# Kernel tuning notes

Hardware: AMD Instinct MI355X
Metric: run time of the kernel (lower is better)

## Reference

```python
import jax, jax.numpy as jnp
import numpy as np

DIM = 128     # channels c (== LayerNorm dim); divisible by HEADS so qk_dim == dim
HEADS = 4
HIDDEN = 256  # dim * mlp_ratio (2.0)
B, H, W = 4, 128, 128


def setup_inputs() -> dict:
    key = jax.random.key(0)
    ks = jax.random.split(key, 8)
    d, hd = DIM, HIDDEN
    return {
        "x": jax.random.normal(ks[0], (B, d, H, W), jnp.float32),
        "ln1_g": jnp.ones((d,), jnp.float32),
        "ln1_b": jnp.zeros((d,), jnp.float32),
        "w_qkv": jax.random.normal(ks[1], (d, 3 * d), jnp.float32) * 0.02,
        "w_out": jax.random.normal(ks[2], (d, d), jnp.float32) * 0.02,
        "b_out": jnp.zeros((d,), jnp.float32),
        "ln2_g": jnp.ones((d,), jnp.float32),
        "ln2_b": jnp.zeros((d,), jnp.float32),
        "w_p0": jax.random.normal(ks[3], (d, hd), jnp.float32) * 0.02,
        "b_p0": jnp.zeros((hd,), jnp.float32),
        "dw_k": jax.random.normal(ks[4], (hd, 1, 5, 5), jnp.float32) * 0.1,
        "bn_g": jnp.ones((hd,), jnp.float32),
        "bn_b": jnp.zeros((hd,), jnp.float32),
        "w_p2": jax.random.normal(ks[5], (hd, d), jnp.float32) * 0.02,
        "b_p2": jnp.zeros((d,), jnp.float32),
        "region_size": 16,
    }


def _ln(x, g, b, eps=1e-5):
    m = x.mean(-1, keepdims=True)
    v = ((x - m) ** 2).mean(-1, keepdims=True)
    return (x - m) * jax.lax.rsqrt(v + eps) * g + b


def _forward(x, ln1_g, ln1_b, w_qkv, w_out, b_out, ln2_g, ln2_b,
             w_p0, b_p0, dw_k, bn_g, bn_b, w_p2, b_p2, region_size):
    b, c, h, w = x.shape
    rs = int(region_size)
    step = rs - 2
    # H,W chosen so pad_h = pad_w = 0 and (H - rs) % step == 0 -> full coverage
    n_r = (h - rs) // step + 1                      # regions per spatial axis (9)
    n = n_r * n_r                                   # total regions (81)
    starts = jnp.arange(n_r) * step
    hh = starts[:, None] + jnp.arange(rs)           # (n_r, rs) row indices
    ih = hh[:, None, :, None]                       # (n_r,1,rs,1)
    iw = hh[None, :, None, :]                       # (1,n_r,1,rs)

    # --- RegionPartitioner: overlapping windowed gather ---
    reg = x[:, :, ih, iw]                           # (b,c,n_r,n_r,rs,rs)
    # rearrange 'b n c h w -> (b n) (h w) c'
    tok = reg.transpose(0, 2, 3, 4, 5, 1).reshape(b * n, rs * rs, c)

    # --- PreNorm AdaptiveAttention + residual ---
    y = _ln(tok, ln1_g, ln1_b)
    qkv = y @ w_qkv                                 # (bn, s, 3c)
    q, k, v = jnp.split(qkv, 3, axis=-1)
    hd = c // HEADS
    split = lambda t: t.reshape(b * n, rs * rs, HEADS, hd).transpose(0, 2, 1, 3)
    q, k, v = split(q), split(k), split(v)
    attn = jax.nn.softmax(jnp.einsum('bhqd,bhkd->bhqk', q, k) * (hd ** -0.5), axis=-1)
    o = jnp.einsum('bhqk,bhkd->bhqd', attn, v)
    o = o.transpose(0, 2, 1, 3).reshape(b * n, rs * rs, c)
    tok = (o @ w_out + b_out) + tok

    # --- RegionIntegrator: overlap-add scatter + count normalize ---
    reg2 = tok.reshape(b, n_r, n_r, rs, rs, c).transpose(0, 5, 1, 2, 3, 4)  # (b,c,nr,nr,rs,rs)
    out = jnp.zeros((b, c, h, w), x.dtype).at[:, :, ih, iw].add(reg2)
    cnt = jnp.zeros((h, w), x.dtype).at[ih, iw].add(
        jnp.ones((n_r, n_r, rs, rs), x.dtype))
    merged = out / jnp.clip(cnt, 1e-8, None)[None, None]

    # --- PreNorm ConvMLP + residual ---
    xf = merged.transpose(0, 2, 3, 1).reshape(b, h * w, c)
    y = _ln(xf, ln2_g, ln2_b)
    y = y @ w_p0 + b_p0                              # (b, hw, hidden)
    ym = y.transpose(0, 2, 1).reshape(b, HIDDEN, h, w)
    ym = jax.lax.conv_general_dilated(
        ym, dw_k, window_strides=(1, 1), padding=[(2, 2), (2, 2)],
        feature_group_count=HIDDEN, dimension_numbers=('NCHW', 'OIHW', 'NCHW'))
    # BatchNorm2d (training-mode batch statistics, biased var, eps=1e-5)
    mu = ym.mean(axis=(0, 2, 3), keepdims=True)
    var = ((ym - mu) ** 2).mean(axis=(0, 2, 3), keepdims=True)
    ym = (ym - mu) * jax.lax.rsqrt(var + 1e-5) * bn_g[None, :, None, None] + bn_b[None, :, None, None]
    ym = jax.nn.gelu(ym, approximate=False)
    y = ym.reshape(b, HIDDEN, h * w).transpose(0, 2, 1)
    y = jax.nn.gelu(y, approximate=False)           # proj[1]
    y = y @ w_p2 + b_p2                              # proj[2]
    y = y + xf
    return y.reshape(b, h, w, c).transpose(0, 3, 1, 2)


def reference(x, ln1_g, ln1_b, w_qkv, w_out, b_out, ln2_g, ln2_b,
              w_p0, b_p0, dw_k, bn_g, bn_b, w_p2, b_p2, region_size):
    return _forward(x, ln1_g, ln1_b, w_qkv, w_out, b_out, ln2_g, ln2_b,
                    w_p0, b_p0, dw_k, bn_g, bn_b, w_p2, b_p2, region_size)
```

## Files before the change

### kernel.cpp

```cpp
#include <hip/hip_runtime.h>

#define DIMC 128
#define NHEADS 4
#define HD 32
#define HID 256
#define BB 4
#define HH_ 128
#define WW_ 128
#define HW 16384
#define RS 16
#define STEP 14
#define NR 9
#define NREGB 81
#define NREG 324
#define TT 256

typedef unsigned short bfu;
typedef __attribute__((ext_vector_type(8))) short bf16x8;
typedef __attribute__((ext_vector_type(4))) float f32x4;

__device__ __forceinline__ float bf2f(bfu u) {
  return __uint_as_float(((unsigned int)u) << 16);
}
__device__ __forceinline__ unsigned cvt_pk_bf16(float lo, float hi) {
  unsigned r;
  asm("v_cvt_pk_bf16_f32 %0, %1, %2" : "=v"(r) : "v"(lo), "v"(hi));
  return r;
}
__device__ __forceinline__ float gelu_fast(float x) {
  float x2 = x * x;
  float z = x * fmaf(x2, 0.07135481627f, 1.5957691216f);
  float e = __expf(-z);
  return __fdividef(x, 1.0f + e);
}

__global__ __launch_bounds__(256) void k1_gather(
    const float* __restrict__ x, const float* __restrict__ g,
    const float* __restrict__ bia, bfu* __restrict__ tok,
    bfu* __restrict__ aln, const float* __restrict__ wqkv,
    const float* __restrict__ wp0, const float* __restrict__ wp2,
    const float* __restrict__ wout, bfu* __restrict__ wqkvT,
    bfu* __restrict__ ap0, bfu* __restrict__ ap2, bfu* __restrict__ awout,
    float* __restrict__ bnacc) {
  int bid = blockIdx.x;
  int tid = threadIdx.x;
  if (bid >= NREG) {
    int pb = bid - NREG;
    if (pb < 24) {
      int task = pb * 256 + tid;
      int kg = task / 384, n = task % 384;
      float v[8];
      #pragma unroll
      for (int j = 0; j < 8; ++j) v[j] = wqkv[(kg * 8 + j) * 384 + n];
      uint4 pk = make_uint4(cvt_pk_bf16(v[0], v[1]), cvt_pk_bf16(v[2], v[3]),
                            cvt_pk_bf16(v[4], v[5]), cvt_pk_bf16(v[6], v[7]));
      *(uint4*)&wqkvT[(size_t)kg * 3072 + n * 8] = pk;
    } else if (pb == 24) {
      bnacc[tid] = 0.f;
      bnacc[256 + tid] = 0.f;
    } else if (pb < 41) {
      int task = (pb - 25) * 256 + tid;
      int kg = task >> 8, f = task & 255;
      float v[8];
      #pragma unroll
      for (int j = 0; j < 8; ++j) v[j] = wp0[(kg * 8 + j) * 256 + f];
      uint4 pk = make_uint4(cvt_pk_bf16(v[0], v[1]), cvt_pk_bf16(v[2], v[3]),
                            cvt_pk_bf16(v[4], v[5]), cvt_pk_bf16(v[6], v[7]));
      *(uint4*)&ap0[((size_t)kg * 256 + f) * 8] = pk;
    } else if (pb < 57) {
      int task = (pb - 41) * 256 + tid;
      int kg = task >> 7, c = task & 127;
      float v[8];
      #pragma unroll
      for (int j = 0; j < 8; ++j) v[j] = wp2[(kg * 8 + j) * 128 + c];
      uint4 pk = make_uint4(cvt_pk_bf16(v[0], v[1]), cvt_pk_bf16(v[2], v[3]),
                            cvt_pk_bf16(v[4], v[5]), cvt_pk_bf16(v[6], v[7]));
      *(uint4*)&ap2[((size_t)kg * 128 + c) * 8] = pk;
    } else {
      int task = (pb - 57) * 256 + tid;
      int kg = task >> 7, c = task & 127;
      float v[8];
      #pragma unroll
      for (int j = 0; j < 8; ++j) v[j] = wout[(kg * 8 + j) * 128 + c];
      uint4 pk = make_uint4(cvt_pk_bf16(v[0], v[1]), cvt_pk_bf16(v[2], v[3]),
                            cvt_pk_bf16(v[4], v[5]), cvt_pk_bf16(v[6], v[7]));
      *(uint4*)&awout[((size_t)kg * 128 + c) * 8] = pk;
    }
    return;
  }
  int reg = bid;
  int b = reg / NREGB, ij = reg % NREGB;
  int i = ij / NR, j = ij % NR;
  int t = tid;
  int r = t >> 4, s = t & 15;
  int hh = i * STEP + r, ww = j * STEP + s;
  const float* xp = x + (size_t)b * DIMC * HW + (size_t)hh * WW_ + ww;
  bfu* tp = tok + (size_t)reg * DIMC * TT + t;
  float sum = 0.f, sq = 0.f;
  #pragma unroll 4
  for (int c = 0; c < DIMC; c += 2) {
    float v0 = xp[(size_t)c * HW];
    float v1 = xp[(size_t)(c + 1) * HW];
    unsigned pk = cvt_pk_bf16(v0, v1);
    tp[c * TT] = (bfu)pk;
    tp[(c + 1) * TT] = (bfu)(pk >> 16);
    sum += v0 + v1;
    sq = fmaf(v0, v0, sq);
    sq = fmaf(v1, v1, sq);
  }
  float mu = sum * (1.0f / DIMC);
  float var = sq * (1.0f / DIMC) - mu * mu;
  float rstd = rsqrtf(var + 1e-5f);
  bfu* ap = aln + (size_t)reg * 32768 + t * 8;
  #pragma unroll
  for (int gidx = 0; gidx < 16; ++gidx) {
    float y[8];
    #pragma unroll
    for (int jj = 0; jj < 8; ++jj) {
      int c = gidx * 8 + jj;
      float vv = xp[(size_t)c * HW];
      y[jj] = (vv - mu) * rstd * g[c] + bia[c];
    }
    uint4 pk = make_uint4(cvt_pk_bf16(y[0], y[1]), cvt_pk_bf16(y[2], y[3]),
                          cvt_pk_bf16(y[4], y[5]), cvt_pk_bf16(y[6], y[7]));
    *(uint4*)&ap[(size_t)gidx * 2048] = pk;
  }
}

__global__ __launch_bounds__(256) void k23_fused(
    const bfu* __restrict__ aln, const bfu* __restrict__ wqkvT,
    bfu* __restrict__ o) {
  int reg = blockIdx.x;
  int h = blockIdx.y;
  __shared__ __align__(16) bfu sQ[256 * 40];
  __shared__ __align__(16) bfu sK[256 * 40];
  __shared__ __align__(16) bfu vperm[8 * 4 * 264];
  int tid = threadIdx.x;
  int wave = tid >> 6, lane = tid & 63;
  int quad = lane >> 4, n16 = lane & 15;

  const bfu* ab = aln + (size_t)reg * 32768 + (wave * 64 + n16) * 8;
  int colb[6];
  colb[0] = h * 32;
  colb[1] = h * 32 + 16;
  colb[2] = 128 + h * 32;
  colb[3] = 144 + h * 32;
  colb[4] = 256 + h * 32;
  colb[5] = 272 + h * 32;
  f32x4 acc[4][6];
  #pragma unroll
  for (int m = 0; m < 4; ++m)
    #pragma unroll
    for (int nt = 0; nt < 6; ++nt) acc[m][nt] = (f32x4){0.f, 0.f, 0.f, 0.f};
  #pragma unroll
  for (int ph = 0; ph < 4; ++ph) {
    int gg = ph * 4 + quad;
    bf16x8 af[4];
    #pragma unroll
    for (int m = 0; m < 4; ++m)
      af[m] = *(const bf16x8*)&ab[(size_t)gg * 2048 + m * 128];
    const bfu* bgg = wqkvT + (size_t)gg * 3072;
    bf16x8 bfr[6];
    #pragma unroll
    for (int nt = 0; nt < 6; ++nt)
      bfr[nt] = *(const bf16x8*)&bgg[(colb[nt] + n16) * 8];
    #pragma unroll
    for (int m = 0; m < 4; ++m)
      #pragma unroll
      for (int nt = 0; nt < 6; ++nt)
        acc[m][nt] =
            __builtin_amdgcn_mfma_f32_16x16x32_bf16(af[m], bfr[nt], acc[m][nt], 0, 0, 0);
  }
  #pragma unroll
  for (int m = 0; m < 4; ++m) {
    int g = wave * 2 + (m >> 1);
    int jt = (m & 1) * 4;
    int T0 = wave * 64 + m * 16 + quad * 4;
    unsigned q00 = cvt_pk_bf16(acc[m][0][0], acc[m][0][1]);
    unsigned q01 = cvt_pk_bf16(acc[m][0][2], acc[m][0][3]);
    unsigned q10 = cvt_pk_bf16(acc[m][1][0], acc[m][1][1]);
    unsigned q11 = cvt_pk_bf16(acc[m][1][2], acc[m][1][3]);
    unsigned k00 = cvt_pk_bf16(acc[m][2][0], acc[m][2][1]);
    unsigned k01 = cvt_pk_bf16(acc[m][2][2], acc[m][2][3]);
    unsigned k10 = cvt_pk_bf16(acc[m][3][0], acc[m][3][1]);
    unsigned k11 = cvt_pk_bf16(acc[m][3][2], acc[m][3][3]);
    sQ[(T0 + 0) * 40 + n16] = (bfu)q00;
    sQ[(T0 + 1) * 40 + n16] = (bfu)(q00 >> 16);
    sQ[(T0 + 2) * 40 + n16] = (bfu)q01;
    sQ[(T0 + 3) * 40 + n16] = (bfu)(q01 >> 16);
    sQ[(T0 + 0) * 40 + 16 + n16] = (bfu)q10;
    sQ[(T0 + 1) * 40 + 16 + n16] = (bfu)(q10 >> 16);
    sQ[(T0 + 2) * 40 + 16 + n16] = (bfu)q11;
    sQ[(T0 + 3) * 40 + 16 + n16] = (bfu)(q11 >> 16);
    sK[(T0 + 0) * 40 + n16] = (bfu)k00;
    sK[(T0 + 1) * 40 + n16] = (bfu)(k00 >> 16);
    sK[(T0 + 2) * 40 + n16] = (bfu)k01;
    sK[(T0 + 3) * 40 + n16] = (bfu)(k01 >> 16);
    sK[(T0 + 0) * 40 + 16 + n16] = (bfu)k10;
    sK[(T0 + 1) * 40 + 16 + n16] = (bfu)(k10 >> 16);
    sK[(T0 + 2) * 40 + 16 + n16] = (bfu)k11;
    sK[(T0 + 3) * 40 + 16 + n16] = (bfu)(k11 >> 16);
    unsigned v0 = cvt_pk_bf16(acc[m][4][0], acc[m][4][1]);
    unsigned v1 = cvt_pk_bf16(acc[m][4][2], acc[m][4][3]);
    unsigned v2 = cvt_pk_bf16(acc[m][5][0], acc[m][5][1]);
    unsigned v3 = cvt_pk_bf16(acc[m][5][2], acc[m][5][3]);
    int vbase = (g * 4 + quad) * 264 + jt;
    *(uint2*)&vperm[vbase + n16 * 8] = make_uint2(v0, v1);
    *(uint2*)&vperm[vbase + (16 + n16) * 8] = make_uint2(v2, v3);
  }
  __syncthreads();

  const f32x4 zero = {0.f, 0.f, 0.f, 0.f};
  const float scale = 0.17677669529663687f;
  for (int mi = 0; mi < 4; ++mi) {
    int mt = wave * 4 + mi;
    bf16x8 qf = *(const bf16x8*)&sQ[(mt * 16 + n16) * 40 + quad * 8];
    f32x4 st[16];
    #pragma unroll
    for (int T = 0; T < 16; ++T) {
      bf16x8 kf = *(const bf16x8*)&sK[(T * 16 + n16) * 40 + quad * 8];
      st[T] = __builtin_amdgcn_mfma_f32_16x16x32_bf16(kf, qf, zero, 0, 0, 0);
    }
    float m = st[0][0];
    #pragma unroll
    for (int T = 0; T < 16; ++T)
      #pragma unroll
      for (int r = 0; r < 4; ++r) m = fmaxf(m, st[T][r]);
    m = fmaxf(m, __shfl_xor(m, 16, 64));
    m = fmaxf(m, __shfl_xor(m, 32, 64));
    float l = 0.f;
    #pragma unroll
    for (int T = 0; T < 16; ++T)
      #pragma unroll
      for (int r = 0; r < 4; ++r) {
        float p = __expf((st[T][r] - m) * scale);
        st[T][r] = p;
        l += p;
      }
    l += __shfl_xor(l, 16, 64);
    l += __shfl_xor(l, 32, 64);
    float inv = 1.0f / l;
    f32x4 oa0 = zero, oa1 = zero;
    #pragma unroll
    for (int g = 0; g < 8; ++g) {
      uint4 pw = make_uint4(cvt_pk_bf16(st[2 * g][0], st[2 * g][1]),
                            cvt_pk_bf16(st[2 * g][2], st[2 * g][3]),
                            cvt_pk_bf16(st[2 * g + 1][0], st[2 * g + 1][1]),
                            cvt_pk_bf16(st[2 * g + 1][2], st[2 * g + 1][3]));
      bf16x8 pf = *(bf16x8*)&pw;
      bf16x8 va = *(const bf16x8*)&vperm[(g * 4 + quad) * 264 + n16 * 8];
      bf16x8 vb = *(const bf16x8*)&vperm[(g * 4 + quad) * 264 + (16 + n16) * 8];
      oa0 = __builtin_amdgcn_mfma_f32_16x16x32_bf16(va, pf, oa0, 0, 0, 0);
      oa1 = __builtin_amdgcn_mfma_f32_16x16x32_bf16(vb, pf, oa1, 0, 0, 0);
    }
    bfu* ob = o + ((size_t)reg * 256 + mt * 16 + n16) * 128 + h * 32 + quad * 4;
    unsigned o0 = cvt_pk_bf16(oa0[0] * inv, oa0[1] * inv);
    unsigned o1 = cvt_pk_bf16(oa0[2] * inv, oa0[3] * inv);
    unsigned o2 = cvt_pk_bf16(oa1[0] * inv, oa1[1] * inv);
    unsigned o3 = cvt_pk_bf16(oa1[2] * inv, oa1[3] * inv);
    *(uint2*)&ob[0] = make_uint2(o0, o1);
    *(uint2*)&ob[16] = make_uint2(o2, o3);
  }
}

__global__ __launch_bounds__(256) void k4_outproj(
    const bfu* __restrict__ o, const bfu* __restrict__ awout,
    const float* __restrict__ bout, bfu* __restrict__ tok) {
  int reg = blockIdx.x;
  int tt = blockIdx.y;
  int tid = threadIdx.x;
  int wave = tid >> 6, lane = tid & 63;
  int quad = lane >> 4, n16 = lane & 15;
  int t = tt * 64 + wave * 16 + n16;
  const bfu* ob = o + ((size_t)reg * 256 + t) * 128;
  f32x4 acc[8];
  #pragma unroll
  for (int mt = 0; mt < 8; ++mt) acc[mt] = (f32x4){0.f, 0.f, 0.f, 0.f};
  #pragma unroll
  for (int kt = 0; kt < 4; ++kt) {
    bf16x8 bfrag = *(const bf16x8*)&ob[kt * 32 + quad * 8];
    const bfu* arow = awout + ((size_t)(kt * 4 + quad) * 128 + n16) * 8;
    #pragma unroll
    for (int mt = 0; mt < 8; ++mt) {
      bf16x8 afrag = *(const bf16x8*)&arow[mt * 128];
      acc[mt] = __builtin_amdgcn_mfma_f32_16x16x32_bf16(afrag, bfrag, acc[mt], 0, 0, 0);
    }
  }
  bfu* tokr = tok + (size_t)reg * DIMC * TT + t;
  #pragma unroll
  for (int mt = 0; mt < 8; ++mt) {
    #pragma unroll
    for (int rp = 0; rp < 2; ++rp) {
      int c = mt * 16 + quad * 4 + rp * 2;
      float v0 = bf2f(tokr[c * TT]) + acc[mt][rp * 2] + bout[c];
      float v1 = bf2f(tokr[(c + 1) * TT]) + acc[mt][rp * 2 + 1] + bout[c + 1];
      unsigned pk = cvt_pk_bf16(v0, v1);
      tokr[c * TT] = (bfu)pk;
      tokr[(c + 1) * TT] = (bfu)(pk >> 16);
    }
  }
}

__global__ __launch_bounds__(512) void k5_merge(
    const bfu* __restrict__ tok, const float* __restrict__ ln2g,
    const float* __restrict__ ln2b, float* __restrict__ xf,
    bfu* __restrict__ xln) {
  int hh = blockIdx.x, b = blockIdx.y;
  int tid = threadIdx.x;
  int w = tid & 127, q = tid >> 7;
  int ilo = (hh >= 2) ? (hh - 2) / 14 : 0;
  int ihi = hh / 14;
  if (ihi > 8) ihi = 8;
  int jlo = (w >= 2) ? (w - 2) / 14 : 0;
  int jhi = w / 14;
  if (jhi > 8) jhi = 8;
  float rcnt = 1.0f / (float)((ihi - ilo + 1) * (jhi - jlo + 1));
  size_t offs[4];
  int nij = 0;
  for (int i = ilo; i <= ihi; ++i)
    for (int j = jlo; j <= jhi; ++j) {
      int reg = b * NREGB + i * NR + j;
      int r = hh - i * STEP, s = w - j * STEP;
      offs[nij++] = (size_t)reg * DIMC * TT + r * 16 + s;
    }
  float* xp = xf + ((size_t)b * DIMC << 14) + hh * WW_ + w;
  float mm[32];
  float sum = 0.f, sq = 0.f;
  int c0 = q * 32;
  for (int cc = 0; cc < 32; ++cc) {
    int c = c0 + cc;
    float s = 0.f;
    for (int k = 0; k < nij; ++k) s += bf2f(tok[offs[k] + c * TT]);
    float m = s * rcnt;
    xp[(size_t)c << 14] = m;
    mm[cc] = m;
    sum += m;
    sq = fmaf(m, m, sq);
  }
  __shared__ float rs[512];
  __shared__ float rq[512];
  __shared__ float muS[128];
  __shared__ float rsdS[128];
  rs[tid] = sum;
  rq[tid] = sq;
  __syncthreads();
  if (tid < 128) {
    float s4 = rs[tid] + rs[tid + 128] + rs[tid + 256] + rs[tid + 384];
    float q4 = rq[tid] + rq[tid + 128] + rq[tid + 256] + rq[tid + 384];
    float mu = s4 * (1.0f / DIMC);
    float var = q4 * (1.0f / DIMC) - mu * mu;
    muS[tid] = mu;
    rsdS[tid] = rsqrtf(var + 1e-5f);
  }
  __syncthreads();
  float mu = muS[w], rstd = rsdS[w];
  int p = hh * WW_ + w;
  #pragma unroll
  for (int gl = 0; gl < 4; ++gl) {
    int gidx = q * 4 + gl;
    float y[8];
    #pragma unroll
    for (int j = 0; j < 8; ++j) {
      int c = gidx * 8 + j;
      y[j] = (mm[gl * 8 + j] - mu) * rstd * ln2g[c] + ln2b[c];
    }
    uint4 pk = make_uint4(cvt_pk_bf16(y[0], y[1]), cvt_pk_bf16(y[2], y[3]),
                          cvt_pk_bf16(y[4], y[5]), cvt_pk_bf16(y[6], y[7]));
    *(uint4*)&xln[(((size_t)(b * 16 + gidx) << 14) + p) * 8] = pk;
  }
}

__global__ __launch_bounds__(256) void k6_p0(
    const bfu* __restrict__ xln, const bfu* __restrict__ ap0,
    const float* __restrict__ bp0, bfu* __restrict__ ym) {
  int b = blockIdx.y;
  int ptile = blockIdx.x * 64;
  int tid = threadIdx.x;
  int wv = tid >> 6, lane = tid & 63;
  int quad = lane >> 4, n16 = lane & 15;
  int p = ptile + wv * 16 + n16;
  f32x4 acc[16];
  #pragma unroll
  for (int mt = 0; mt < 16; ++mt) acc[mt] = (f32x4){0.f, 0.f, 0.f, 0.f};
  #pragma unroll
  for (int ph = 0; ph < 4; ++ph) {
    int gg = ph * 4 + quad;
    bf16x8 bfrag = *(const bf16x8*)&xln[(((size_t)(b * 16 + gg) << 14) + p) * 8];
    const bfu* arow = ap0 + ((size_t)gg * 256 + n16) * 8;
    #pragma unroll
    for (int mt = 0; mt < 16; ++mt) {
      bf16x8 afrag = *(const bf16x8*)&arow[mt * 128];
      acc[mt] = __builtin_amdgcn_mfma_f32_16x16x32_bf16(afrag, bfrag, acc[mt], 0, 0, 0);
    }
  }
  #pragma unroll
  for (int mt = 0; mt < 16; ++mt) {
    #pragma unroll
    for (int rp = 0; rp < 2; ++rp) {
      int f = mt * 16 + quad * 4 + rp * 2;
      float v0 = acc[mt][rp * 2] + bp0[f];
      float v1 = acc[mt][rp * 2 + 1] + bp0[f + 1];
      unsigned pk = cvt_pk_bf16(v0, v1);
      ym[((size_t)(b * HID + f) << 14) + p] = (bfu)pk;
      ym[((size_t)(b * HID + f + 1) << 14) + p] = (bfu)(pk >> 16);
    }
  }
}

__global__ __launch_bounds__(256) void k7_conv(
    const bfu* __restrict__ ym, const float* __restrict__ dwk,
    bfu* __restrict__ ym2, float* __restrict__ bnacc) {
  int bf = blockIdx.x;
  int f = bf & (HID - 1);
  __shared__ bfu sp[128 * 134];
  const bfu* in = ym + ((size_t)bf << 14);
  int tid = threadIdx.x;
  for (int idx = tid; idx < 2048; idx += 256) {
    int r = idx >> 4, c8 = (idx & 15) << 3;
    ushort4 a = *(const ushort4*)&in[(r << 7) + c8];
    ushort4 b = *(const ushort4*)&in[(r << 7) + c8 + 4];
    bfu* d = &sp[r * 134 + c8];
    d[0] = a.x; d[1] = a.y; d[2] = a.z; d[3] = a.w;
    d[4] = b.x; d[5] = b.y; d[6] = b.z; d[7] = b.w;
  }
  float wk[25];
  #pragma unroll
  for (int i = 0; i < 25; ++i) wk[i] = dwk[f * 25 + i];
  __syncthreads();
  int row = tid >> 1, half = (tid & 1) << 6;
  float acc[64];
  #pragma unroll
  for (int i = 0; i < 64; ++i) acc[i] = 0.f;
  #pragma unroll
  for (int ky = 0; ky < 5; ++ky) {
    int y = row + ky - 2;
    if (y < 0 || y >= 128) continue;
    const bfu* rp = &sp[y * 134];
    float win[68];
    #pragma unroll
    for (int c = 0; c < 68; ++c) {
      int cc = half + c - 2;
      win[c] = (cc >= 0 && cc < 128) ? bf2f(rp[cc]) : 0.f;
    }
    #pragma unroll
    for (int kx = 0; kx < 5; ++kx) {
      float wv = wk[ky * 5 + kx];
      #pragma unroll
      for (int i = 0; i < 64; ++i) acc[i] = fmaf(win[i + kx], wv, acc[i]);
    }
  }
  float s = 0.f, sq = 0.f;
  #pragma unroll
  for (int i = 0; i < 64; ++i) {
    s += acc[i];
    sq = fmaf(acc[i], acc[i], sq);
  }
  bfu* op = ym2 + ((size_t)bf << 14) + (row << 7) + half;
  #pragma unroll
  for (int g8 = 0; g8 < 8; ++g8) {
    uint4 pk = make_uint4(cvt_pk_bf16(acc[g8 * 8 + 0], acc[g8 * 8 + 1]),
                          cvt_pk_bf16(acc[g8 * 8 + 2], acc[g8 * 8 + 3]),
                          cvt_pk_bf16(acc[g8 * 8 + 4], acc[g8 * 8 + 5]),
                          cvt_pk_bf16(acc[g8 * 8 + 6], acc[g8 * 8 + 7]));
    *(uint4*)&op[g8 * 8] = pk;
  }
  __syncthreads();
  float* red = (float*)sp;
  red[tid] = s;
  red[256 + tid] = sq;
  __syncthreads();
  for (int o = 128; o > 0; o >>= 1) {
    if (tid < o) {
      red[tid] += red[tid + o];
      red[256 + tid] += red[256 + tid + o];
    }
    __syncthreads();
  }
  if (tid == 0) {
    atomicAdd(&bnacc[f], red[0]);
    atomicAdd(&bnacc[HID + f], red[256]);
  }
}

__global__ __launch_bounds__(256) void k10_p2(
    const bfu* __restrict__ ym2, const float* __restrict__ bnacc,
    const float* __restrict__ bng, const float* __restrict__ bnb,
    const bfu* __restrict__ ap2, const float* __restrict__ bp2,
    const float* __restrict__ xf, float* __restrict__ outp) {
  int b = blockIdx.y;
  int ptile = blockIdx.x * 64;
  int tid = threadIdx.x;
  __shared__ float sA[HID];
  __shared__ float sB[HID];
  {
    float mu = bnacc[tid] * (1.0f / 65536.f);
    float var = bnacc[HID + tid] * (1.0f / 65536.f) - mu * mu;
    float sa = rsqrtf(var + 1e-5f) * bng[tid];
    sA[tid] = sa;
    sB[tid] = bnb[tid] - mu * sa;
  }
  __syncthreads();
  int wv = tid >> 6, lane = tid & 63;
  int quad = lane >> 4, n16 = lane & 15;
  int p = ptile + wv * 16 + n16;
  f32x4 acc[8];
  #pragma unroll
  for (int mt = 0; mt < 8; ++mt) acc[mt] = (f32x4){0.f, 0.f, 0.f, 0.f};
  #pragma unroll
  for (int ph = 0; ph < 8; ++ph) {
    int gg = ph * 4 + quad;
    const bfu* ymp = ym2 + (((size_t)(b * HID + gg * 8)) << 14) + p;
    float vals[8];
    #pragma unroll
    for (int j = 0; j < 8; ++j) vals[j] = bf2f(ymp[(size_t)j << 14]);
    float gv[8];
    #pragma unroll
    for (int j = 0; j < 8; ++j) {
      float v = fmaf(vals[j], sA[gg * 8 + j], sB[gg * 8 + j]);
      gv[j] = gelu_fast(gelu_fast(v));
    }
    uint4 pk = make_uint4(cvt_pk_bf16(gv[0], gv[1]), cvt_pk_bf16(gv[2], gv[3]),
                          cvt_pk_bf16(gv[4], gv[5]), cvt_pk_bf16(gv[6], gv[7]));
    bf16x8 bfrag = *(bf16x8*)&pk;
    const bfu* arow = ap2 + ((size_t)gg * 128 + n16) * 8;
    #pragma unroll
    for (int mt = 0; mt < 8; ++mt) {
      bf16x8 afrag = *(const bf16x8*)&arow[mt * 128];
      acc[mt] = __builtin_amdgcn_mfma_f32_16x16x32_bf16(afrag, bfrag, acc[mt], 0, 0, 0);
    }
  }
  #pragma unroll
  for (int mt = 0; mt < 8; ++mt) {
    #pragma unroll
    for (int r = 0; r < 4; ++r) {
      int c = mt * 16 + quad * 4 + r;
      size_t off = ((size_t)(b * DIMC + c) << 14) + p;
      outp[off] = acc[mt][r] + bp2[c] + xf[off];
    }
  }
}

extern "C" void kernel_launch(void* const* d_in, const int* in_sizes, int n_in,
                              void* d_out, int out_size, void* d_ws,
                              size_t ws_size, hipStream_t stream) {
  const float* x = (const float*)d_in[0];
  const float* ln1_g = (const float*)d_in[1];
  const float* ln1_b = (const float*)d_in[2];
  const float* w_qkv = (const float*)d_in[3];
  const float* w_out = (const float*)d_in[4];
  const float* b_out = (const float*)d_in[5];
  const float* ln2_g = (const float*)d_in[6];
  const float* ln2_b = (const float*)d_in[7];
  const float* w_p0 = (const float*)d_in[8];
  const float* b_p0 = (const float*)d_in[9];
  const float* dw_k = (const float*)d_in[10];
  const float* bn_g = (const float*)d_in[11];
  const float* bn_b = (const float*)d_in[12];
  const float* w_p2 = (const float*)d_in[13];
  const float* b_p2 = (const float*)d_in[14];
  float* outp = (float*)d_out;

  char* ws = (char*)d_ws;
  size_t off = 0;
  auto alloc = [&](size_t bytes) {
    void* p = ws + off;
    off += (bytes + 1023) & ~(size_t)1023;
    return p;
  };
  bfu* tok = (bfu*)alloc((size_t)NREG * DIMC * TT * 2);
  float* xf = (float*)alloc((size_t)BB * DIMC * HW * 4);
  bfu* xln = (bfu*)alloc((size_t)BB * DIMC * HW * 2);
  bfu* ym = (bfu*)alloc((size_t)BB * HID * HW * 2);
  bfu* ym2 = (bfu*)alloc((size_t)BB * HID * HW * 2);
  float* bnacc = (float*)alloc(2 * HID * 4);
  bfu* wqkvT = (bfu*)alloc(16 * 3072 * 2);
  bfu* ap0 = (bfu*)alloc(16 * 256 * 8 * 2);
  bfu* ap2 = (bfu*)alloc(32 * 128 * 8 * 2);
  bfu* awout = (bfu*)alloc(16 * 128 * 8 * 2);
  bfu* o = ym;
  bfu* aln = ym2;

  k1_gather<<<NREG + 65, 256, 0, stream>>>(x, ln1_g, ln1_b, tok, aln, w_qkv,
                                           w_p0, w_p2, w_out, wqkvT, ap0, ap2,
                                           awout, bnacc);
  k23_fused<<<dim3(NREG, NHEADS), 256, 0, stream>>>(aln, wqkvT, o);
  k4_outproj<<<dim3(NREG, 4), 256, 0, stream>>>(o, awout, b_out, tok);
  k5_merge<<<dim3(HH_, BB), 512, 0, stream>>>(tok, ln2_g, ln2_b, xf, xln);
  k6_p0<<<dim3(256, BB), 256, 0, stream>>>(xln, ap0, b_p0, ym);
  k7_conv<<<BB * HID, 256, 0, stream>>>(ym, dw_k, ym2, bnacc);
  k10_p2<<<dim3(256, BB), 256, 0, stream>>>(ym2, bnacc, bn_g, bn_b, ap2, b_p2,
                                            xf, outp);
}
```

Baseline: 326.1 us.

## Switch token buffer to token-major layout with vectorized channel accesses

Changes the tok intermediate from channel-major [reg][c][t] to token-major [reg][t][c] across the gather, output-projection residual, and merge kernels. Each thread now writes 8 bf16 channels as one 16-byte store, does 32-bit read-modify-write in the residual add, and reads uint4 vectors in the merge. The aim is to replace many scalar 2-byte strided accesses with wide vector accesses. The cost is that adjacent lanes now hit addresses 256 bytes apart instead of contiguous ones, so coalescing across the wavefront may suffer.

```diff
diff --git a/kernel.cpp b/kernel.cpp
--- a/kernel.cpp
+++ b/kernel.cpp
@@ -33,6 +33,7 @@
   float e = __expf(-z);
   return __fdividef(x, 1.0f + e);
 }
+
 
 __global__ __launch_bounds__(256) void k1_gather(
     const float* __restrict__ x, const float* __restrict__ g,
@@ -95,18 +96,21 @@
   int r = t >> 4, s = t & 15;
   int hh = i * STEP + r, ww = j * STEP + s;
   const float* xp = x + (size_t)b * DIMC * HW + (size_t)hh * WW_ + ww;
-  bfu* tp = tok + (size_t)reg * DIMC * TT + t;
+  bfu* tp = tok + (size_t)reg * DIMC * TT + (size_t)t * DIMC;
   float sum = 0.f, sq = 0.f;
-  #pragma unroll 4
-  for (int c = 0; c < DIMC; c += 2) {
-    float v0 = xp[(size_t)c * HW];
-    float v1 = xp[(size_t)(c + 1) * HW];
-    unsigned pk = cvt_pk_bf16(v0, v1);
-    tp[c * TT] = (bfu)pk;
-    tp[(c + 1) * TT] = (bfu)(pk >> 16);
-    sum += v0 + v1;
-    sq = fmaf(v0, v0, sq);
-    sq = fmaf(v1, v1, sq);
+  #pragma unroll 2
+  for (int c8 = 0; c8 < DIMC; c8 += 8) {
+    unsigned pks[4];
+    #pragma unroll
+    for (int jj = 0; jj < 4; ++jj) {
+      float v0 = xp[(size_t)(c8 + 2 * jj) * HW];
+      float v1 = xp[(size_t)(c8 + 2 * jj + 1) * HW];
+      pks[jj] = cvt_pk_bf16(v0, v1);
+      sum += v0 + v1;
+      sq = fmaf(v0, v0, sq);
+      sq = fmaf(v1, v1, sq);
+    }
+    *(uint4*)&tp[c8] = make_uint4(pks[0], pks[1], pks[2], pks[3]);
   }
   float mu = sum * (1.0f / DIMC);
   float var = sq * (1.0f / DIMC) - mu * mu;
@@ -286,17 +290,16 @@
       acc[mt] = __builtin_amdgcn_mfma_f32_16x16x32_bf16(afrag, bfrag, acc[mt], 0, 0, 0);
     }
   }
-  bfu* tokr = tok + (size_t)reg * DIMC * TT + t;
+  bfu* tokr = tok + (size_t)reg * DIMC * TT + (size_t)t * DIMC;
   #pragma unroll
   for (int mt = 0; mt < 8; ++mt) {
     #pragma unroll
     for (int rp = 0; rp < 2; ++rp) {
       int c = mt * 16 + quad * 4 + rp * 2;
-      float v0 = bf2f(tokr[c * TT]) + acc[mt][rp * 2] + bout[c];
-      float v1 = bf2f(tokr[(c + 1) * TT]) + acc[mt][rp * 2 + 1] + bout[c + 1];
-      unsigned pk = cvt_pk_bf16(v0, v1);
-      tokr[c * TT] = (bfu)pk;
-      tokr[(c + 1) * TT] = (bfu)(pk >> 16);
+      unsigned old = *(const unsigned*)&tokr[c];
+      float v0 = bf2f((bfu)old) + acc[mt][rp * 2] + bout[c];
+      float v1 = bf2f((bfu)(old >> 16)) + acc[mt][rp * 2 + 1] + bout[c + 1];
+      *(unsigned*)&tokr[c] = cvt_pk_bf16(v0, v1);
     }
   }
 }
@@ -321,21 +324,37 @@
     for (int j = jlo; j <= jhi; ++j) {
       int reg = b * NREGB + i * NR + j;
       int r = hh - i * STEP, s = w - j * STEP;
-      offs[nij++] = (size_t)reg * DIMC * TT + r * 16 + s;
+      offs[nij++] = (size_t)reg * DIMC * TT + (size_t)(r * 16 + s) * DIMC;
     }
   float* xp = xf + ((size_t)b * DIMC << 14) + hh * WW_ + w;
   float mm[32];
   float sum = 0.f, sq = 0.f;
   int c0 = q * 32;
-  for (int cc = 0; cc < 32; ++cc) {
-    int c = c0 + cc;
-    float s = 0.f;
-    for (int k = 0; k < nij; ++k) s += bf2f(tok[offs[k] + c * TT]);
-    float m = s * rcnt;
-    xp[(size_t)c << 14] = m;
-    mm[cc] = m;
-    sum += m;
-    sq = fmaf(m, m, sq);
+  #pragma unroll
+  for (int gl = 0; gl < 4; ++gl) {
+    int cb = c0 + gl * 8;
+    float v[8];
+    #pragma unroll
+    for (int jj = 0; jj < 8; ++jj) v[jj] = 0.f;
+    for (int k = 0; k < nij; ++k) {
+      uint4 u = *(const uint4*)&tok[offs[k] + cb];
+      v[0] += bf2f((bfu)u.x);
+      v[1] += bf2f((bfu)(u.x >> 16));
+      v[2] += bf2f((bfu)u.y);
+      v[3] += bf2f((bfu)(u.y >> 16));
+      v[4] += bf2f((bfu)u.z);
+      v[5] += bf2f((bfu)(u.z >> 16));
+      v[6] += bf2f((bfu)u.w);
+      v[7] += bf2f((bfu)(u.w >> 16));
+    }
+    #pragma unroll
+    for (int jj = 0; jj < 8; ++jj) {
+      float m = v[jj] * rcnt;
+      xp[(size_t)(cb + jj) << 14] = m;
+      mm[gl * 8 + jj] = m;
+      sum += m;
+      sq = fmaf(m, m, sq);
+    }
   }
   __shared__ float rs[512];
   __shared__ float rq[512];
```

New measurement: 309.5 us. 5.1% less time.
